# Performance work log

Hardware: AMD Instinct MI355X
Metric: run time of the kernel (lower is better)

The kernel has to match this reference:

```python
import jax, jax.numpy as jnp
import numpy as np

SEQ, B, IN, H = 256, 64, 512, 1024


def setup_inputs() -> dict:
    key = jax.random.key(0)
    ks = jax.random.split(key, 17)
    s_in = 0.05  # small init to avoid gate saturation
    inp = {"x": jax.random.normal(ks[0], (SEQ, B, IN), dtype=jnp.float32)}
    names = ["f", "i", "o", "c"]
    for j, g in enumerate(names):
        inp[f"W_i{g}"] = jax.random.normal(ks[1 + 4 * j], (H, IN), dtype=jnp.float32) * s_in
        inp[f"b_i{g}"] = jax.random.normal(ks[2 + 4 * j], (H,), dtype=jnp.float32) * s_in
        inp[f"W_h{g}"] = jax.random.normal(ks[3 + 4 * j], (H, H), dtype=jnp.float32) * s_in
        inp[f"b_h{g}"] = jax.random.normal(ks[4 + 4 * j], (H,), dtype=jnp.float32) * s_in
    return inp


def reference(x, W_if, b_if, W_hf, b_hf, W_ii, b_ii, W_hi, b_hi,
              W_io, b_io, W_ho, b_ho, W_ic, b_ic, W_hc, b_hc):
    # Precompute input-to-gate projections for the whole sequence (one big GEMM each)
    xf = jnp.einsum('sbi,hi->sbh', x, W_if) + b_if
    xi = jnp.einsum('sbi,hi->sbh', x, W_ii) + b_ii
    xo = jnp.einsum('sbi,hi->sbh', x, W_io) + b_io
    xc = jnp.einsum('sbi,hi->sbh', x, W_ic) + b_ic

    batch = x.shape[1]
    hidden = W_hf.shape[0]
    h0 = jnp.zeros((batch, hidden), dtype=x.dtype)
    c0 = jnp.zeros((batch, hidden), dtype=x.dtype)

    def step(carry, xs):
        h, c = carry
        xf_t, xi_t, xo_t, xc_t = xs
        f = jax.nn.sigmoid(xf_t + h @ W_hf.T + b_hf)
        i = jax.nn.sigmoid(xi_t + h @ W_hi.T + b_hi)
        o = jax.nn.sigmoid(xo_t + h @ W_ho.T + b_ho)
        g = jnp.tanh(xc_t + h @ W_hc.T + b_hc)
        c_new = f * c + i * g
        h_new = o * jnp.tanh(c_new)
        return (h_new, c_new), h_new

    (h_fin, c_fin), h_seq = jax.lax.scan(step, (h0, c0), (xf, xi, xo, xc))
    # match torch module's (1, B, H) leading layer dim on final states
    return h_seq, h_fin[None], c_fin[None]
```

## Files before the change

kernel.cpp:

```cpp
#include <hip/hip_runtime.h>
#include <hip/hip_bf16.h>

typedef __bf16 bf16_t;
typedef __bf16 bf16x8 __attribute__((ext_vector_type(8)));
typedef float f32x4 __attribute__((ext_vector_type(4)));
typedef int   i32x4 __attribute__((ext_vector_type(4)));

#define SEQLEN 256
#define NBATCH 64
#define INDIM  512
#define HID    1024
#define NBLK   256

#define XF_OFF   0ull
#define WXF_OFF  16777216ull
#define WHF_OFF  20971520ull
#define BS_OFF   29360128ull
#define HSEQ_OFF 29376512ull
#define FLG_OFF  63062016ull
#define SLOT_BYTES 131072ull

__device__ __forceinline__ bf16x8 cvt8(float4 a, float4 b) {
  bf16x8 v;
  v[0] = (bf16_t)a.x; v[1] = (bf16_t)a.y; v[2] = (bf16_t)a.z; v[3] = (bf16_t)a.w;
  v[4] = (bf16_t)b.x; v[5] = (bf16_t)b.y; v[6] = (bf16_t)b.z; v[7] = (bf16_t)b.w;
  return v;
}

__global__ __launch_bounds__(256) void pack_xf_k(const float* __restrict__ x,
                                                 bf16_t* __restrict__ xf) {
  int idx = blockIdx.x * 256 + threadIdx.x;
  int t = idx >> 12;
  int r = idx & 4095;
  int batch = r >> 6, c8 = r & 63;
  const float4* s = (const float4*)(x + ((size_t)t * NBATCH + batch) * INDIM + c8 * 8);
  int kk = c8 >> 2, lhi = c8 & 3;
  int kh = kk >> 3, kkl = kk & 7;
  int bg = batch >> 4, lane = (batch & 15) + 16 * lhi;
  bf16_t* d = xf + (size_t)t * 32768 + (size_t)(((bg * 2 + kh) * 8 + kkl) * 64 + lane) * 8;
  *(bf16x8*)d = cvt8(s[0], s[1]);
}

struct GatePtrs {
  const float* Wi[4];
  const float* bi[4];
  const float* Wh[4];
  const float* bh[4];
};

__global__ __launch_bounds__(256) void pack_w_k(GatePtrs p,
                                                bf16_t* __restrict__ Wxf,
                                                bf16_t* __restrict__ Whf,
                                                float* __restrict__ bsum) {
  int idx = blockIdx.x * 256 + threadIdx.x;
  int row = idx / 192;
  int c   = idx % 192;
  int blk = row >> 5, r32 = row & 31, g = r32 >> 3, jj = r32 & 7;
  int j = blk * 8 + jj;
  int g2 = r32 >> 4, lrow = r32 & 15;
  if (c == 0) bsum[row] = p.bi[g][j] + p.bh[g][j];
  if (c < 64) {
    const float4* s = (const float4*)(p.Wi[g] + (size_t)j * INDIM + c * 8);
    int kk = c >> 2, lane = lrow + 16 * (c & 3);
    *(bf16x8*)(Wxf + (size_t)blk * 16384 + (size_t)((kk * 2 + g2) * 64 + lane) * 8) = cvt8(s[0], s[1]);
  } else {
    int cc = c - 64;
    const float4* s = (const float4*)(p.Wh[g] + (size_t)j * HID + cc * 8);
    int kk = cc >> 2, lane = lrow + 16 * (cc & 3);
    *(bf16x8*)(Whf + (size_t)blk * 32768 + (size_t)((kk * 2 + g2) * 64 + lane) * 8) = cvt8(s[0], s[1]);
  }
}

#define PLDC(dst, ptr, OFF) \
  asm volatile("global_load_dwordx4 %0, %1, off offset:" OFF : "=v"(dst) : "v"(ptr))

__global__ __launch_bounds__(256, 1) void lstm_rec_k(const bf16_t* __restrict__ Whf,
                                                     const bf16_t* __restrict__ Wxf,
                                                     const bf16_t* __restrict__ xf,
                                                     const float* __restrict__ bsum,
                                                     bf16_t* __restrict__ hseq,
                                                     int* __restrict__ flags,
                                                     float* __restrict__ out) {
  const int b = blockIdx.x;
  const int cb = b & 127, bgs = b >> 7;
  const int tid = threadIdx.x;
  const int w = tid >> 6, l = tid & 63;
  const int bhalf = w >> 1, kh = w & 1;
  const int bg = bgs * 2 + bhalf;

  __shared__ bf16_t wlds[49152];
  __shared__ float  accbuf[2][32][36];

  {
    const bf16_t* whb = Whf + (size_t)cb * 32768;
    const bf16_t* wxb = Wxf + (size_t)cb * 16384;
#pragma unroll
    for (int i = 0; i < 16; ++i)
      __builtin_amdgcn_global_load_lds((const __attribute__((address_space(1))) void*)(whb + (i * 256 + tid) * 8),
                                       (__attribute__((address_space(3))) void*)(wlds + (i * 256 + tid) * 8),
                                       16, 0, 0);
#pragma unroll
    for (int i = 0; i < 8; ++i)
      __builtin_amdgcn_global_load_lds((const __attribute__((address_space(1))) void*)(wxb + (i * 256 + tid) * 8),
                                       (__attribute__((address_space(3))) void*)(wlds + 32768 + (i * 256 + tid) * 8),
                                       16, 0, 0);
  }

  const int eb = tid >> 3, ejj = tid & 7;
  const int gb = bgs * 32 + eb;
  const int j  = cb * 8 + ejj;
  const int p_lane = (gb & 15) + 16 * ((j & 31) >> 3);
  const int p_kkg = j >> 5;
  const size_t pub_off = (size_t)((((gb >> 4) * 2 + (p_kkg >> 4)) * 16 + (p_kkg & 15)) * 64 + p_lane) * 16
                       + (size_t)(j & 7) * 2;
  const float bsF = bsum[cb * 32 + ejj];
  const float bsI = bsum[cb * 32 + 8 + ejj];
  const float bsO = bsum[cb * 32 + 16 + ejj];
  const float bsC = bsum[cb * 32 + 24 + ejj];
  float cs = 0.f;

  const size_t pollbase = (size_t)((bg * 2 + kh) * 16) * 1024 + (size_t)l * 16;
  const char* fbase = (const char*)flags + (size_t)l * 16;

  __syncthreads();

  for (int t = 0; t < SEQLEN; ++t) {
    const bf16_t* xfe = xf + (size_t)t * 32768 + (size_t)((bg * 2 + kh) * 8 * 64 + l) * 8;
    const char* xp0 = (const char*)xfe;
    const char* xp1 = xp0 + 4096;
    i32x4 xr[8];
    PLDC(xr[0], xp0, "0"); PLDC(xr[1], xp0, "1024"); PLDC(xr[2], xp0, "2048"); PLDC(xr[3], xp0, "3072");
    PLDC(xr[4], xp1, "0"); PLDC(xr[5], xp1, "1024"); PLDC(xr[6], xp1, "2048"); PLDC(xr[7], xp1, "3072");

    if (t) {
      const char* fp = fbase + (size_t)t * 1024;
      i32x4 f;
      for (;;) {
        asm volatile("global_load_dwordx4 %0, %1, off sc0 sc1" : "=v"(f) : "v"(fp));
        asm volatile("s_waitcnt vmcnt(0)" ::: "memory");
        if (!__any((f[0] == 0) | (f[1] == 0) | (f[2] == 0) | (f[3] == 0))) break;
        __builtin_amdgcn_s_sleep(1);
      }
    }
    asm volatile("" ::: "memory");

    const char* q0 = (const char*)hseq + (size_t)t * SLOT_BYTES + pollbase;
    const char* q1 = q0 + 4096;
    const char* q2 = q0 + 8192;
    const char* q3 = q0 + 12288;
    i32x4 hv[16];
    PLDC(hv[0],  q0, "0"); PLDC(hv[1],  q0, "1024"); PLDC(hv[2],  q0, "2048"); PLDC(hv[3],  q0, "3072");
    PLDC(hv[4],  q1, "0"); PLDC(hv[5],  q1, "1024"); PLDC(hv[6],  q1, "2048"); PLDC(hv[7],  q1, "3072");
    PLDC(hv[8],  q2, "0"); PLDC(hv[9],  q2, "1024"); PLDC(hv[10], q2, "2048"); PLDC(hv[11], q2, "3072");
    PLDC(hv[12], q3, "0"); PLDC(hv[13], q3, "1024"); PLDC(hv[14], q3, "2048"); PLDC(hv[15], q3, "3072");
    asm volatile("s_waitcnt vmcnt(0)" ::: "memory");
    __builtin_amdgcn_sched_barrier(0);

    f32x4 acc0 = {}, acc1 = {};
#pragma unroll
    for (int kkl = 0; kkl < 16; ++kkl) {
      const int kk = kh * 16 + kkl;
      bf16x8 hf = __builtin_bit_cast(bf16x8, hv[kkl]);
      bf16x8 w0 = *(const bf16x8*)(wlds + (size_t)((kk * 2 + 0) * 64 + l) * 8);
      bf16x8 w1 = *(const bf16x8*)(wlds + (size_t)((kk * 2 + 1) * 64 + l) * 8);
      acc0 = __builtin_amdgcn_mfma_f32_16x16x32_bf16(hf, w0, acc0, 0, 0, 0);
      acc1 = __builtin_amdgcn_mfma_f32_16x16x32_bf16(hf, w1, acc1, 0, 0, 0);
    }
#pragma unroll
    for (int kkl = 0; kkl < 8; ++kkl) {
      const int kk = kh * 8 + kkl;
      bf16x8 xv = __builtin_bit_cast(bf16x8, xr[kkl]);
      bf16x8 w0 = *(const bf16x8*)(wlds + 32768 + (size_t)((kk * 2 + 0) * 64 + l) * 8);
      bf16x8 w1 = *(const bf16x8*)(wlds + 32768 + (size_t)((kk * 2 + 1) * 64 + l) * 8);
      acc0 = __builtin_amdgcn_mfma_f32_16x16x32_bf16(xv, w0, acc0, 0, 0, 0);
      acc1 = __builtin_amdgcn_mfma_f32_16x16x32_bf16(xv, w1, acc1, 0, 0, 0);
    }

    *(f32x4*)&accbuf[kh][l & 15][bhalf * 16 + (l >> 4) * 4]        = acc0;
    *(f32x4*)&accbuf[kh][16 + (l & 15)][bhalf * 16 + (l >> 4) * 4] = acc1;
    __syncthreads();

    {
      float pf = bsF + accbuf[0][ejj][eb]      + accbuf[1][ejj][eb];
      float pi = bsI + accbuf[0][8 + ejj][eb]  + accbuf[1][8 + ejj][eb];
      float po = bsO + accbuf[0][16 + ejj][eb] + accbuf[1][16 + ejj][eb];
      float pc = bsC + accbuf[0][24 + ejj][eb] + accbuf[1][24 + ejj][eb];
      float fg = 1.f / (1.f + __expf(-pf));
      float ig = 1.f / (1.f + __expf(-pi));
      float og = 1.f / (1.f + __expf(-po));
      float e2 = __expf(-2.f * fabsf(pc));
      float gg = __builtin_copysignf((1.f - e2) / (1.f + e2), pc);
      cs = fg * cs + ig * gg;
      float e2c = __expf(-2.f * fabsf(cs));
      float th = __builtin_copysignf((1.f - e2c) / (1.f + e2c), cs);
      float hval = og * th;

      out[((size_t)t * NBATCH + gb) * HID + j] = hval;
      unsigned int my = (unsigned int)__builtin_bit_cast(unsigned short, (bf16_t)hval);
      unsigned int other = __shfl_xor(my, 1);
      if (!(tid & 1)) {
        unsigned int pk = my | (other << 16);
        unsigned int* hd = (unsigned int*)((char*)hseq + (size_t)(t + 1) * SLOT_BYTES + pub_off);
        __hip_atomic_store(hd, pk, __ATOMIC_RELAXED, __HIP_MEMORY_SCOPE_AGENT);
      }
      if (t == SEQLEN - 1) {
        out[(size_t)SEQLEN * NBATCH * HID + (size_t)gb * HID + j] = hval;
        out[(size_t)SEQLEN * NBATCH * HID + (size_t)NBATCH * HID + (size_t)gb * HID + j] = cs;
      }
    }

    __syncthreads();
    if (t < SEQLEN - 1 && tid == 0)
      __hip_atomic_store(&flags[(t + 1) * NBLK + b], 1, __ATOMIC_RELAXED, __HIP_MEMORY_SCOPE_AGENT);
  }
}

extern "C" void kernel_launch(void* const* d_in, const int* in_sizes, int n_in,
                              void* d_out, int out_size, void* d_ws, size_t ws_size,
                              hipStream_t stream) {
  (void)in_sizes; (void)n_in; (void)out_size; (void)ws_size;
  char* ws = (char*)d_ws;
  bf16_t* xf   = (bf16_t*)(ws + XF_OFF);
  bf16_t* Wxf  = (bf16_t*)(ws + WXF_OFF);
  bf16_t* Whf  = (bf16_t*)(ws + WHF_OFF);
  float*  bs   = (float*)(ws + BS_OFF);
  bf16_t* hseq = (bf16_t*)(ws + HSEQ_OFF);
  int*    flg  = (int*)(ws + FLG_OFF);

  const float* x = (const float*)d_in[0];
  GatePtrs p;
  for (int g = 0; g < 4; ++g) {
    p.Wi[g] = (const float*)d_in[1 + 4 * g];
    p.bi[g] = (const float*)d_in[2 + 4 * g];
    p.Wh[g] = (const float*)d_in[3 + 4 * g];
    p.bh[g] = (const float*)d_in[4 + 4 * g];
  }

  pack_xf_k<<<4096, 256, 0, stream>>>(x, xf);
  pack_w_k<<<3072, 256, 0, stream>>>(p, Wxf, Whf, bs);
  hipMemsetAsync(flg, 0, 257 * NBLK * 4, stream);
  hipMemsetAsync(hseq, 0, SLOT_BYTES, stream);
  lstm_rec_k<<<NBLK, 256, 0, stream>>>(Whf, Wxf, xf, bs, hseq, flg, (float*)d_out);
}
```

Baseline: 861.9 us.

## Hold recurrent weights in registers and overlap x-projection MFMAs with h loads

The recurrent weight slice now lives in VGPRs (32 dwordx4 per lane), loaded once before the loop, instead of being read from LDS every step. The input-projection MFMAs run first behind a partial vmcnt wait, so they overlap the h-state loads, and the recurrent MFMAs start only after those loads arrive. The global store of the output sequence is moved after the flag publish so it is off the inter-block critical path. A padding LDS array keeps occupancy at one block per CU. The cost is much higher register pressure, which risks spills.

```diff
diff --git a/kernel.cpp b/kernel.cpp
--- a/kernel.cpp
+++ b/kernel.cpp
@@ -88,23 +88,36 @@
   const int bhalf = w >> 1, kh = w & 1;
   const int bg = bgs * 2 + bhalf;
 
-  __shared__ bf16_t wlds[49152];
+  __shared__ bf16_t xwlds[16384];
   __shared__ float  accbuf[2][32][36];
-
+  __shared__ char   ldspad[45056];
+
+  if (tid > 1000000) ((volatile char*)ldspad)[0] = 1;
+
+#pragma unroll
+  for (int i = 0; i < 8; ++i)
+    __builtin_amdgcn_global_load_lds((const __attribute__((address_space(1))) void*)(Wxf + (size_t)cb * 16384 + (i * 256 + tid) * 8),
+                                     (__attribute__((address_space(3))) void*)(xwlds + (i * 256 + tid) * 8),
+                                     16, 0, 0);
+
+  i32x4 whr[16][2];
   {
-    const bf16_t* whb = Whf + (size_t)cb * 32768;
-    const bf16_t* wxb = Wxf + (size_t)cb * 16384;
-#pragma unroll
-    for (int i = 0; i < 16; ++i)
-      __builtin_amdgcn_global_load_lds((const __attribute__((address_space(1))) void*)(whb + (i * 256 + tid) * 8),
-                                       (__attribute__((address_space(3))) void*)(wlds + (i * 256 + tid) * 8),
-                                       16, 0, 0);
-#pragma unroll
-    for (int i = 0; i < 8; ++i)
-      __builtin_amdgcn_global_load_lds((const __attribute__((address_space(1))) void*)(wxb + (i * 256 + tid) * 8),
-                                       (__attribute__((address_space(3))) void*)(wlds + 32768 + (i * 256 + tid) * 8),
-                                       16, 0, 0);
-  }
+    const char* wb = (const char*)Whf + (size_t)cb * 65536 + (size_t)(kh * 32768) + (size_t)l * 16;
+    const char* w0 = wb;          const char* w1 = wb + 4096;
+    const char* w2 = wb + 8192;   const char* w3 = wb + 12288;
+    const char* w4 = wb + 16384;  const char* w5 = wb + 20480;
+    const char* w6 = wb + 24576;  const char* w7 = wb + 28672;
+    PLDC(whr[0][0],  w0, "0"); PLDC(whr[0][1],  w0, "1024"); PLDC(whr[1][0],  w0, "2048"); PLDC(whr[1][1],  w0, "3072");
+    PLDC(whr[2][0],  w1, "0"); PLDC(whr[2][1],  w1, "1024"); PLDC(whr[3][0],  w1, "2048"); PLDC(whr[3][1],  w1, "3072");
+    PLDC(whr[4][0],  w2, "0"); PLDC(whr[4][1],  w2, "1024"); PLDC(whr[5][0],  w2, "2048"); PLDC(whr[5][1],  w2, "3072");
+    PLDC(whr[6][0],  w3, "0"); PLDC(whr[6][1],  w3, "1024"); PLDC(whr[7][0],  w3, "2048"); PLDC(whr[7][1],  w3, "3072");
+    PLDC(whr[8][0],  w4, "0"); PLDC(whr[8][1],  w4, "1024"); PLDC(whr[9][0],  w4, "2048"); PLDC(whr[9][1],  w4, "3072");
+    PLDC(whr[10][0], w5, "0"); PLDC(whr[10][1], w5, "1024"); PLDC(whr[11][0], w5, "2048"); PLDC(whr[11][1], w5, "3072");
+    PLDC(whr[12][0], w6, "0"); PLDC(whr[12][1], w6, "1024"); PLDC(whr[13][0], w6, "2048"); PLDC(whr[13][1], w6, "3072");
+    PLDC(whr[14][0], w7, "0"); PLDC(whr[14][1], w7, "1024"); PLDC(whr[15][0], w7, "2048"); PLDC(whr[15][1], w7, "3072");
+  }
+  asm volatile("s_waitcnt vmcnt(0)" ::: "memory");
+  __builtin_amdgcn_sched_barrier(0);
 
   const int eb = tid >> 3, ejj = tid & 7;
   const int gb = bgs * 32 + eb;
@@ -125,8 +138,7 @@
   __syncthreads();
 
   for (int t = 0; t < SEQLEN; ++t) {
-    const bf16_t* xfe = xf + (size_t)t * 32768 + (size_t)((bg * 2 + kh) * 8 * 64 + l) * 8;
-    const char* xp0 = (const char*)xfe;
+    const char* xp0 = (const char*)xf + (size_t)t * 65536 + (size_t)((bg * 2 + kh) * 8 * 64 + l) * 16;
     const char* xp1 = xp0 + 4096;
     i32x4 xr[8];
     PLDC(xr[0], xp0, "0"); PLDC(xr[1], xp0, "1024"); PLDC(xr[2], xp0, "2048"); PLDC(xr[3], xp0, "3072");
@@ -153,33 +165,34 @@
     PLDC(hv[4],  q1, "0"); PLDC(hv[5],  q1, "1024"); PLDC(hv[6],  q1, "2048"); PLDC(hv[7],  q1, "3072");
     PLDC(hv[8],  q2, "0"); PLDC(hv[9],  q2, "1024"); PLDC(hv[10], q2, "2048"); PLDC(hv[11], q2, "3072");
     PLDC(hv[12], q3, "0"); PLDC(hv[13], q3, "1024"); PLDC(hv[14], q3, "2048"); PLDC(hv[15], q3, "3072");
-    asm volatile("s_waitcnt vmcnt(0)" ::: "memory");
+
+    asm volatile("s_waitcnt vmcnt(16)" ::: "memory");
     __builtin_amdgcn_sched_barrier(0);
-
     f32x4 acc0 = {}, acc1 = {};
-#pragma unroll
-    for (int kkl = 0; kkl < 16; ++kkl) {
-      const int kk = kh * 16 + kkl;
-      bf16x8 hf = __builtin_bit_cast(bf16x8, hv[kkl]);
-      bf16x8 w0 = *(const bf16x8*)(wlds + (size_t)((kk * 2 + 0) * 64 + l) * 8);
-      bf16x8 w1 = *(const bf16x8*)(wlds + (size_t)((kk * 2 + 1) * 64 + l) * 8);
-      acc0 = __builtin_amdgcn_mfma_f32_16x16x32_bf16(hf, w0, acc0, 0, 0, 0);
-      acc1 = __builtin_amdgcn_mfma_f32_16x16x32_bf16(hf, w1, acc1, 0, 0, 0);
-    }
 #pragma unroll
     for (int kkl = 0; kkl < 8; ++kkl) {
       const int kk = kh * 8 + kkl;
       bf16x8 xv = __builtin_bit_cast(bf16x8, xr[kkl]);
-      bf16x8 w0 = *(const bf16x8*)(wlds + 32768 + (size_t)((kk * 2 + 0) * 64 + l) * 8);
-      bf16x8 w1 = *(const bf16x8*)(wlds + 32768 + (size_t)((kk * 2 + 1) * 64 + l) * 8);
+      bf16x8 w0 = *(const bf16x8*)(xwlds + (size_t)((kk * 2 + 0) * 64 + l) * 8);
+      bf16x8 w1 = *(const bf16x8*)(xwlds + (size_t)((kk * 2 + 1) * 64 + l) * 8);
       acc0 = __builtin_amdgcn_mfma_f32_16x16x32_bf16(xv, w0, acc0, 0, 0, 0);
       acc1 = __builtin_amdgcn_mfma_f32_16x16x32_bf16(xv, w1, acc1, 0, 0, 0);
+    }
+
+    asm volatile("s_waitcnt vmcnt(0)" ::: "memory");
+    __builtin_amdgcn_sched_barrier(0);
+#pragma unroll
+    for (int kkl = 0; kkl < 16; ++kkl) {
+      bf16x8 hf = __builtin_bit_cast(bf16x8, hv[kkl]);
+      acc0 = __builtin_amdgcn_mfma_f32_16x16x32_bf16(hf, __builtin_bit_cast(bf16x8, whr[kkl][0]), acc0, 0, 0, 0);
+      acc1 = __builtin_amdgcn_mfma_f32_16x16x32_bf16(hf, __builtin_bit_cast(bf16x8, whr[kkl][1]), acc1, 0, 0, 0);
     }
 
     *(f32x4*)&accbuf[kh][l & 15][bhalf * 16 + (l >> 4) * 4]        = acc0;
     *(f32x4*)&accbuf[kh][16 + (l & 15)][bhalf * 16 + (l >> 4) * 4] = acc1;
     __syncthreads();
 
+    float hval;
     {
       float pf = bsF + accbuf[0][ejj][eb]      + accbuf[1][ejj][eb];
       float pi = bsI + accbuf[0][8 + ejj][eb]  + accbuf[1][8 + ejj][eb];
@@ -193,9 +206,8 @@
       cs = fg * cs + ig * gg;
       float e2c = __expf(-2.f * fabsf(cs));
       float th = __builtin_copysignf((1.f - e2c) / (1.f + e2c), cs);
-      float hval = og * th;
-
-      out[((size_t)t * NBATCH + gb) * HID + j] = hval;
+      hval = og * th;
+
       unsigned int my = (unsigned int)__builtin_bit_cast(unsigned short, (bf16_t)hval);
       unsigned int other = __shfl_xor(my, 1);
       if (!(tid & 1)) {
@@ -203,15 +215,17 @@
         unsigned int* hd = (unsigned int*)((char*)hseq + (size_t)(t + 1) * SLOT_BYTES + pub_off);
         __hip_atomic_store(hd, pk, __ATOMIC_RELAXED, __HIP_MEMORY_SCOPE_AGENT);
       }
-      if (t == SEQLEN - 1) {
-        out[(size_t)SEQLEN * NBATCH * HID + (size_t)gb * HID + j] = hval;
-        out[(size_t)SEQLEN * NBATCH * HID + (size_t)NBATCH * HID + (size_t)gb * HID + j] = cs;
-      }
     }
 
     __syncthreads();
     if (t < SEQLEN - 1 && tid == 0)
       __hip_atomic_store(&flags[(t + 1) * NBLK + b], 1, __ATOMIC_RELAXED, __HIP_MEMORY_SCOPE_AGENT);
+
+    out[((size_t)t * NBATCH + gb) * HID + j] = hval;
+    if (t == SEQLEN - 1) {
+      out[(size_t)SEQLEN * NBATCH * HID + (size_t)gb * HID + j] = hval;
+      out[(size_t)SEQLEN * NBATCH * HID + (size_t)NBATCH * HID + (size_t)gb * HID + j] = cs;
+    }
   }
 }
 
```

After: 736.8 us. -14.5%, faster.
